# Performance work log

Measured on AMD Instinct MI355X. Metric: run time of the kernel, lower is better.

## Reference

```python
import jax, jax.numpy as jnp
import numpy as np

N_NODES = 50000
N_EDGES = 640000
IN_CH, HID_CH, OUT_CH = 128, 128, 40


def setup_inputs() -> dict:
    key = jax.random.key(0)
    k1, k2, k3, k4 = jax.random.split(key, 4)
    x = jax.random.normal(k1, (N_NODES, IN_CH), dtype=jnp.float32)
    edge_index = jax.random.randint(k2, (2, N_EDGES), 0, N_NODES, dtype=jnp.int64)
    # Glorot-ish scaled weights
    W1 = jax.random.normal(k3, (IN_CH, HID_CH), dtype=jnp.float32) * (1.0 / np.sqrt(IN_CH))
    b1 = jnp.zeros((HID_CH,), dtype=jnp.float32)
    W2 = jax.random.normal(k4, (HID_CH, OUT_CH), dtype=jnp.float32) * (1.0 / np.sqrt(HID_CH))
    b2 = jnp.zeros((OUT_CH,), dtype=jnp.float32)
    return {"x": x, "edge_index": edge_index, "W1": W1, "b1": b1, "W2": W2, "b2": b2}


def gcn_conv(x, src, dst, W, b, n_nodes):
    """PyG-style GCNConv: self-loops + symmetric normalization + linear + bias.
    src/dst already include self-loop edges."""
    deg = jax.ops.segment_sum(jnp.ones_like(dst, dtype=x.dtype), dst, num_segments=n_nodes)
    dinv = jnp.where(deg > 0, jax.lax.rsqrt(deg), 0.0)          # deg^{-1/2}, 0 for isolated
    norm = dinv[src] * dinv[dst]                                 # [E+N]
    xw = x @ W                                                   # [N, F_out] dense GEMM
    msgs = xw[src] * norm[:, None]                               # gather + scale  [E+N, F_out]
    agg = jax.ops.segment_sum(msgs, dst, num_segments=n_nodes)   # scatter-add
    return agg + b


def reference(x, edge_index, W1, b1, W2, b2):
    n_nodes = x.shape[0]
    loops = jnp.arange(n_nodes, dtype=edge_index.dtype)
    src = jnp.concatenate([edge_index[0], loops])
    dst = jnp.concatenate([edge_index[1], loops])
    h = jax.nn.relu(gcn_conv(x, src, dst, W1, b1, n_nodes))
    # dropout is identity in eval mode (deterministic reference)
    return gcn_conv(h, src, dst, W2, b2, n_nodes)
```

## Files before the change

kernel.cpp:

```cpp
#include <hip/hip_runtime.h>
#include <cstdint>

#define NN 50000
#define NE 640000
#define NFILL 625
#define MB1 782

typedef unsigned short ushort_t;

__device__ __forceinline__ ushort_t f2bf(float f) {
    unsigned int b = __float_as_uint(f);
    return (ushort_t)((b + 0x7FFF + ((b >> 16) & 1)) >> 16);
}
__device__ __forceinline__ float bf2f(ushort_t u) {
    return __uint_as_float(((unsigned int)u) << 16);
}


__global__ void hist_kernel(const int* __restrict__ dst, int* __restrict__ cnt) {
    int tid = blockIdx.x * 256 + threadIdx.x;
#pragma unroll
    for (int k = 0; k < 4; ++k) {
        int e = tid + k * 160000;
        atomicAdd(&cnt[dst[e]], 1);
    }
}

__global__ void scan_block(const int* __restrict__ in, int* __restrict__ out,
                           int* __restrict__ partials, int n) {
    __shared__ int sm[256];
    int t = threadIdx.x;
    int gid = blockIdx.x * 256 + t;
    int v = (gid < n) ? in[gid] : 0;
    sm[t] = v;
    __syncthreads();
#pragma unroll
    for (int off = 1; off < 256; off <<= 1) {
        int add = (t >= off) ? sm[t - off] : 0;
        __syncthreads();
        sm[t] += add;
        __syncthreads();
    }
    if (gid < n) out[gid] = sm[t] - v;
    if (t == 255) partials[blockIdx.x] = sm[255];
}

__global__ void scan_partials(int* __restrict__ p, int nb) {
    __shared__ int sm[256];
    int t = threadIdx.x;
    int v = (t < nb) ? p[t] : 0;
    sm[t] = v;
    __syncthreads();
#pragma unroll
    for (int off = 1; off < 256; off <<= 1) {
        int add = (t >= off) ? sm[t - off] : 0;
        __syncthreads();
        sm[t] += add;
        __syncthreads();
    }
    if (t < nb) p[t] = sm[t] - v;
}

__global__ void finalize_offsets(int* __restrict__ offs, const int* __restrict__ partials,
                                 int* __restrict__ cursor, const int* __restrict__ cnt,
                                 float* __restrict__ dinv, int n) {
    int gid = blockIdx.x * 256 + threadIdx.x;
    if (gid < n) {
        int v = offs[gid] + partials[blockIdx.x];
        offs[gid] = v;
        cursor[gid] = v;
        dinv[gid] = rsqrtf((float)cnt[gid] + 1.0f);
    }
}


__global__ __launch_bounds__(256) void fused_fill_gemm(const int* __restrict__ ei,
                                                       int* __restrict__ cursor,
                                                       ushort_t* __restrict__ csr_src,
                                                       const float* __restrict__ A,
                                                       const float* __restrict__ B,
                                                       const float* __restrict__ dinv,
                                                       ushort_t* __restrict__ C,
                                                       int M, int N) {
    __shared__ float As[64][68];
    __shared__ __align__(16) float Bs[64][64];

    if (blockIdx.x < NFILL) {
        int tid = blockIdx.x * 256 + threadIdx.x;
#pragma unroll
        for (int k = 0; k < 4; ++k) {
            int e = tid + k * 160000;
            int s = ei[e], d = ei[NE + e];
            int pos = atomicAdd(&cursor[d], 1);
            csr_src[pos] = (ushort_t)s;
        }
        return;
    }

    const int b  = blockIdx.x - NFILL;
    const int t  = threadIdx.x;
    const int m0 = (b % MB1) * 64;
    const int n0 = (b / MB1) * 64;
    const int tx = t & 15, ty = t >> 4;

    float acc[4][4] = {};

    for (int ks = 0; ks < 2; ++ks) {
#pragma unroll
        for (int i = 0; i < 4; ++i) {
            int idx = i * 256 + t;
            int r = idx >> 4, c4 = idx & 15;
            int gm = m0 + r;
            float4 v = make_float4(0.f, 0.f, 0.f, 0.f);
            if (gm < M) v = *reinterpret_cast<const float4*>(&A[(size_t)gm * 128 + ks * 64 + c4 * 4]);
            As[r][c4 * 4 + 0] = v.x;
            As[r][c4 * 4 + 1] = v.y;
            As[r][c4 * 4 + 2] = v.z;
            As[r][c4 * 4 + 3] = v.w;
        }
#pragma unroll
        for (int i = 0; i < 4; ++i) {
            int idx = i * 256 + t;
            int k = idx >> 4, c4 = idx & 15;
            int gk = ks * 64 + k;
            int gn = n0 + c4 * 4;
            float4 v;
            v.x = (gn + 0 < N) ? B[(size_t)gk * N + gn + 0] : 0.f;
            v.y = (gn + 1 < N) ? B[(size_t)gk * N + gn + 1] : 0.f;
            v.z = (gn + 2 < N) ? B[(size_t)gk * N + gn + 2] : 0.f;
            v.w = (gn + 3 < N) ? B[(size_t)gk * N + gn + 3] : 0.f;
            *reinterpret_cast<float4*>(&Bs[k][c4 * 4]) = v;
        }
        __syncthreads();

#pragma unroll 8
        for (int k = 0; k < 64; ++k) {
            float a0 = As[ty * 4 + 0][k];
            float a1 = As[ty * 4 + 1][k];
            float a2 = As[ty * 4 + 2][k];
            float a3 = As[ty * 4 + 3][k];
            float4 bb = *reinterpret_cast<const float4*>(&Bs[k][tx * 4]);
            acc[0][0] += a0 * bb.x; acc[0][1] += a0 * bb.y; acc[0][2] += a0 * bb.z; acc[0][3] += a0 * bb.w;
            acc[1][0] += a1 * bb.x; acc[1][1] += a1 * bb.y; acc[1][2] += a1 * bb.z; acc[1][3] += a1 * bb.w;
            acc[2][0] += a2 * bb.x; acc[2][1] += a2 * bb.y; acc[2][2] += a2 * bb.z; acc[2][3] += a2 * bb.w;
            acc[3][0] += a3 * bb.x; acc[3][1] += a3 * bb.y; acc[3][2] += a3 * bb.z; acc[3][3] += a3 * bb.w;
        }
        __syncthreads();
    }

#pragma unroll
    for (int i = 0; i < 4; ++i) {
        int gm = m0 + ty * 4 + i;
        if (gm >= M) continue;
        float s = dinv[gm];
        int gn = n0 + tx * 4;
        if (gn + 3 < N) {
            ushort4 o;
            o.x = f2bf(acc[i][0] * s); o.y = f2bf(acc[i][1] * s);
            o.z = f2bf(acc[i][2] * s); o.w = f2bf(acc[i][3] * s);
            *reinterpret_cast<ushort4*>(&C[(size_t)gm * N + gn]) = o;
        } else {
#pragma unroll
            for (int j = 0; j < 4; ++j)
                if (gn + j < N) C[(size_t)gm * N + gn + j] = f2bf(acc[i][j] * s);
        }
    }
}


__global__ __launch_bounds__(256) void gemm_k128_scaled(const float* __restrict__ A,
                                                        const float* __restrict__ B,
                                                        const float* __restrict__ dinv,
                                                        ushort_t* __restrict__ C,
                                                        int M, int N) {
    __shared__ float As[64][68];
    __shared__ __align__(16) float Bs[64][64];
    const int t  = threadIdx.x;
    const int m0 = blockIdx.x * 64;
    const int n0 = blockIdx.y * 64;
    const int tx = t & 15, ty = t >> 4;

    float acc[4][4] = {};

    for (int ks = 0; ks < 2; ++ks) {
#pragma unroll
        for (int i = 0; i < 4; ++i) {
            int idx = i * 256 + t;
            int r = idx >> 4, c4 = idx & 15;
            int gm = m0 + r;
            float4 v = make_float4(0.f, 0.f, 0.f, 0.f);
            if (gm < M) v = *reinterpret_cast<const float4*>(&A[(size_t)gm * 128 + ks * 64 + c4 * 4]);
            As[r][c4 * 4 + 0] = v.x;
            As[r][c4 * 4 + 1] = v.y;
            As[r][c4 * 4 + 2] = v.z;
            As[r][c4 * 4 + 3] = v.w;
        }
#pragma unroll
        for (int i = 0; i < 4; ++i) {
            int idx = i * 256 + t;
            int k = idx >> 4, c4 = idx & 15;
            int gk = ks * 64 + k;
            int gn = n0 + c4 * 4;
            float4 v;
            v.x = (gn + 0 < N) ? B[(size_t)gk * N + gn + 0] : 0.f;
            v.y = (gn + 1 < N) ? B[(size_t)gk * N + gn + 1] : 0.f;
            v.z = (gn + 2 < N) ? B[(size_t)gk * N + gn + 2] : 0.f;
            v.w = (gn + 3 < N) ? B[(size_t)gk * N + gn + 3] : 0.f;
            *reinterpret_cast<float4*>(&Bs[k][c4 * 4]) = v;
        }
        __syncthreads();

#pragma unroll 8
        for (int k = 0; k < 64; ++k) {
            float a0 = As[ty * 4 + 0][k];
            float a1 = As[ty * 4 + 1][k];
            float a2 = As[ty * 4 + 2][k];
            float a3 = As[ty * 4 + 3][k];
            float4 bb = *reinterpret_cast<const float4*>(&Bs[k][tx * 4]);
            acc[0][0] += a0 * bb.x; acc[0][1] += a0 * bb.y; acc[0][2] += a0 * bb.z; acc[0][3] += a0 * bb.w;
            acc[1][0] += a1 * bb.x; acc[1][1] += a1 * bb.y; acc[1][2] += a1 * bb.z; acc[1][3] += a1 * bb.w;
            acc[2][0] += a2 * bb.x; acc[2][1] += a2 * bb.y; acc[2][2] += a2 * bb.z; acc[2][3] += a2 * bb.w;
            acc[3][0] += a3 * bb.x; acc[3][1] += a3 * bb.y; acc[3][2] += a3 * bb.z; acc[3][3] += a3 * bb.w;
        }
        __syncthreads();
    }

#pragma unroll
    for (int i = 0; i < 4; ++i) {
        int gm = m0 + ty * 4 + i;
        if (gm >= M) continue;
        float s = dinv[gm];
        int gn = n0 + tx * 4;
        if (gn + 3 < N) {
            ushort4 o;
            o.x = f2bf(acc[i][0] * s); o.y = f2bf(acc[i][1] * s);
            o.z = f2bf(acc[i][2] * s); o.w = f2bf(acc[i][3] * s);
            *reinterpret_cast<ushort4*>(&C[(size_t)gm * N + gn]) = o;
        } else {
#pragma unroll
            for (int j = 0; j < 4; ++j)
                if (gn + j < N) C[(size_t)gm * N + gn + j] = f2bf(acc[i][j] * s);
        }
    }
}


__global__ __launch_bounds__(256) void gather128(const int* __restrict__ offs,
                                                 const int* __restrict__ ends,
                                                 const ushort_t* __restrict__ csr_src,
                                                 const ushort_t* __restrict__ Hs,
                                                 const float* __restrict__ dinv,
                                                 const float* __restrict__ b1,
                                                 float* __restrict__ h) {
    const int c = (threadIdx.x & 31) * 4;
    const int n = (blockIdx.x * 256 + threadIdx.x) >> 5;
    const int beg = offs[n], end = ends[n];
    float4 acc = make_float4(0.f, 0.f, 0.f, 0.f);
    int j = beg;
    const int n4end = beg + ((end - beg) & ~3);
    for (; j < n4end; j += 4) {
        int s0 = csr_src[j + 0], s1 = csr_src[j + 1];
        int s2 = csr_src[j + 2], s3 = csr_src[j + 3];
        ushort4 v0 = *reinterpret_cast<const ushort4*>(Hs + (size_t)s0 * 128 + c);
        ushort4 v1 = *reinterpret_cast<const ushort4*>(Hs + (size_t)s1 * 128 + c);
        ushort4 v2 = *reinterpret_cast<const ushort4*>(Hs + (size_t)s2 * 128 + c);
        ushort4 v3 = *reinterpret_cast<const ushort4*>(Hs + (size_t)s3 * 128 + c);
        acc.x += bf2f(v0.x) + bf2f(v1.x) + bf2f(v2.x) + bf2f(v3.x);
        acc.y += bf2f(v0.y) + bf2f(v1.y) + bf2f(v2.y) + bf2f(v3.y);
        acc.z += bf2f(v0.z) + bf2f(v1.z) + bf2f(v2.z) + bf2f(v3.z);
        acc.w += bf2f(v0.w) + bf2f(v1.w) + bf2f(v2.w) + bf2f(v3.w);
    }
    for (; j < end; ++j) {
        int s = csr_src[j];
        ushort4 v = *reinterpret_cast<const ushort4*>(Hs + (size_t)s * 128 + c);
        acc.x += bf2f(v.x); acc.y += bf2f(v.y);
        acc.z += bf2f(v.z); acc.w += bf2f(v.w);
    }
    float di = dinv[n];
    ushort4 sv = *reinterpret_cast<const ushort4*>(Hs + (size_t)n * 128 + c);
    float4 bv = *reinterpret_cast<const float4*>(b1 + c);
    float4 r;
    r.x = fmaxf(fmaf(di, acc.x + bf2f(sv.x), bv.x), 0.f);
    r.y = fmaxf(fmaf(di, acc.y + bf2f(sv.y), bv.y), 0.f);
    r.z = fmaxf(fmaf(di, acc.z + bf2f(sv.z), bv.z), 0.f);
    r.w = fmaxf(fmaf(di, acc.w + bf2f(sv.w), bv.w), 0.f);
    *reinterpret_cast<float4*>(h + (size_t)n * 128 + c) = r;
}


__global__ __launch_bounds__(256) void gather40(const int* __restrict__ offs,
                                                const int* __restrict__ ends,
                                                const ushort_t* __restrict__ csr_src,
                                                const ushort_t* __restrict__ Hs,
                                                const float* __restrict__ dinv,
                                                const float* __restrict__ b2,
                                                float* __restrict__ out) {
    int idx = blockIdx.x * 256 + threadIdx.x;
    if (idx >= NN * 10) return;
    const int n = idx / 10;
    const int c = (idx - n * 10) * 4;
    const int beg = offs[n], end = ends[n];
    float4 acc = make_float4(0.f, 0.f, 0.f, 0.f);
    int j = beg;
    const int n4end = beg + ((end - beg) & ~3);
    for (; j < n4end; j += 4) {
        int s0 = csr_src[j + 0], s1 = csr_src[j + 1];
        int s2 = csr_src[j + 2], s3 = csr_src[j + 3];
        ushort4 v0 = *reinterpret_cast<const ushort4*>(Hs + (size_t)s0 * 40 + c);
        ushort4 v1 = *reinterpret_cast<const ushort4*>(Hs + (size_t)s1 * 40 + c);
        ushort4 v2 = *reinterpret_cast<const ushort4*>(Hs + (size_t)s2 * 40 + c);
        ushort4 v3 = *reinterpret_cast<const ushort4*>(Hs + (size_t)s3 * 40 + c);
        acc.x += bf2f(v0.x) + bf2f(v1.x) + bf2f(v2.x) + bf2f(v3.x);
        acc.y += bf2f(v0.y) + bf2f(v1.y) + bf2f(v2.y) + bf2f(v3.y);
        acc.z += bf2f(v0.z) + bf2f(v1.z) + bf2f(v2.z) + bf2f(v3.z);
        acc.w += bf2f(v0.w) + bf2f(v1.w) + bf2f(v2.w) + bf2f(v3.w);
    }
    for (; j < end; ++j) {
        int s = csr_src[j];
        ushort4 v = *reinterpret_cast<const ushort4*>(Hs + (size_t)s * 40 + c);
        acc.x += bf2f(v.x); acc.y += bf2f(v.y);
        acc.z += bf2f(v.z); acc.w += bf2f(v.w);
    }
    float di = dinv[n];
    ushort4 sv = *reinterpret_cast<const ushort4*>(Hs + (size_t)n * 40 + c);
    float4 bv = *reinterpret_cast<const float4*>(b2 + c);
    float4 r;
    r.x = fmaf(di, acc.x + bf2f(sv.x), bv.x);
    r.y = fmaf(di, acc.y + bf2f(sv.y), bv.y);
    r.z = fmaf(di, acc.z + bf2f(sv.z), bv.z);
    r.w = fmaf(di, acc.w + bf2f(sv.w), bv.w);
    *reinterpret_cast<float4*>(out + (size_t)n * 40 + c) = r;
}


extern "C" void kernel_launch(void* const* d_in, const int* in_sizes, int n_in,
                              void* d_out, int out_size, void* d_ws, size_t ws_size,
                              hipStream_t stream) {
    const float* x  = (const float*)d_in[0];
    const int*   ei = (const int*)d_in[1];
    const float* W1 = (const float*)d_in[2];
    const float* b1 = (const float*)d_in[3];
    const float* W2 = (const float*)d_in[4];
    const float* b2 = (const float*)d_in[5];
    float* out = (float*)d_out;

    int*      deg_i    = (int*)d_ws;
    float*    dinv     = (float*)d_ws + 50048;
    int*      offs     = (int*)d_ws + 100096;
    int*      cursor   = (int*)d_ws + 150144;
    int*      partials = (int*)d_ws + 200192;
    ushort_t* csr_src  = (ushort_t*)((int*)d_ws + 200704);
    ushort_t* H1b      = (ushort_t*)((int*)d_ws + 520704);
    float*    h        = (float*)d_ws + 3720704;
    ushort_t* H2b      = H1b;

    const int NB = (NN + 255) / 256;

    hipMemsetAsync(deg_i, 0, NN * sizeof(int), stream);
    hist_kernel<<<625, 256, 0, stream>>>(ei + NE, deg_i);
    scan_block<<<NB, 256, 0, stream>>>(deg_i, offs, partials, NN);
    scan_partials<<<1, 256, 0, stream>>>(partials, NB);
    finalize_offsets<<<NB, 256, 0, stream>>>(offs, partials, cursor, deg_i, dinv, NN);

    fused_fill_gemm<<<NFILL + MB1 * 2, 256, 0, stream>>>(ei, cursor, csr_src,
                                                         x, W1, dinv, H1b, NN, 128);

    gather128<<<NN * 32 / 256, 256, 0, stream>>>(offs, cursor, csr_src, H1b, dinv, b1, h);

    gemm_k128_scaled<<<dim3(MB1, 1), 256, 0, stream>>>(h, W2, dinv, H2b, NN, 40);
    gather40<<<(NN * 10 + 255) / 256, 256, 0, stream>>>(offs, cursor, csr_src, H2b, dinv, b2, out);
}
```

Before: 230.4 us.

## Replace CSR build with fixed-width ELL adjacency, dropping histogram and scan passes

```diff
diff --git a/kernel.cpp b/kernel.cpp
--- a/kernel.cpp
+++ b/kernel.cpp
@@ -3,6 +3,7 @@
 
 #define NN 50000
 #define NE 640000
+#define ELLW 64
 #define NFILL 625
 #define MB1 782
 
@@ -17,69 +18,11 @@
 }
 
 
-__global__ void hist_kernel(const int* __restrict__ dst, int* __restrict__ cnt) {
-    int tid = blockIdx.x * 256 + threadIdx.x;
-#pragma unroll
-    for (int k = 0; k < 4; ++k) {
-        int e = tid + k * 160000;
-        atomicAdd(&cnt[dst[e]], 1);
-    }
-}
-
-__global__ void scan_block(const int* __restrict__ in, int* __restrict__ out,
-                           int* __restrict__ partials, int n) {
-    __shared__ int sm[256];
-    int t = threadIdx.x;
-    int gid = blockIdx.x * 256 + t;
-    int v = (gid < n) ? in[gid] : 0;
-    sm[t] = v;
-    __syncthreads();
-#pragma unroll
-    for (int off = 1; off < 256; off <<= 1) {
-        int add = (t >= off) ? sm[t - off] : 0;
-        __syncthreads();
-        sm[t] += add;
-        __syncthreads();
-    }
-    if (gid < n) out[gid] = sm[t] - v;
-    if (t == 255) partials[blockIdx.x] = sm[255];
-}
-
-__global__ void scan_partials(int* __restrict__ p, int nb) {
-    __shared__ int sm[256];
-    int t = threadIdx.x;
-    int v = (t < nb) ? p[t] : 0;
-    sm[t] = v;
-    __syncthreads();
-#pragma unroll
-    for (int off = 1; off < 256; off <<= 1) {
-        int add = (t >= off) ? sm[t - off] : 0;
-        __syncthreads();
-        sm[t] += add;
-        __syncthreads();
-    }
-    if (t < nb) p[t] = sm[t] - v;
-}
-
-__global__ void finalize_offsets(int* __restrict__ offs, const int* __restrict__ partials,
-                                 int* __restrict__ cursor, const int* __restrict__ cnt,
-                                 float* __restrict__ dinv, int n) {
-    int gid = blockIdx.x * 256 + threadIdx.x;
-    if (gid < n) {
-        int v = offs[gid] + partials[blockIdx.x];
-        offs[gid] = v;
-        cursor[gid] = v;
-        dinv[gid] = rsqrtf((float)cnt[gid] + 1.0f);
-    }
-}
-
-
 __global__ __launch_bounds__(256) void fused_fill_gemm(const int* __restrict__ ei,
                                                        int* __restrict__ cursor,
-                                                       ushort_t* __restrict__ csr_src,
+                                                       ushort_t* __restrict__ ell,
                                                        const float* __restrict__ A,
                                                        const float* __restrict__ B,
-                                                       const float* __restrict__ dinv,
                                                        ushort_t* __restrict__ C,
                                                        int M, int N) {
     __shared__ float As[64][68];
@@ -92,7 +35,7 @@
             int e = tid + k * 160000;
             int s = ei[e], d = ei[NE + e];
             int pos = atomicAdd(&cursor[d], 1);
-            csr_src[pos] = (ushort_t)s;
+            ell[(size_t)d * ELLW + pos] = (ushort_t)s;
         }
         return;
     }
@@ -152,25 +95,39 @@
     for (int i = 0; i < 4; ++i) {
         int gm = m0 + ty * 4 + i;
         if (gm >= M) continue;
-        float s = dinv[gm];
         int gn = n0 + tx * 4;
         if (gn + 3 < N) {
             ushort4 o;
-            o.x = f2bf(acc[i][0] * s); o.y = f2bf(acc[i][1] * s);
-            o.z = f2bf(acc[i][2] * s); o.w = f2bf(acc[i][3] * s);
+            o.x = f2bf(acc[i][0]); o.y = f2bf(acc[i][1]);
+            o.z = f2bf(acc[i][2]); o.w = f2bf(acc[i][3]);
             *reinterpret_cast<ushort4*>(&C[(size_t)gm * N + gn]) = o;
         } else {
 #pragma unroll
             for (int j = 0; j < 4; ++j)
-                if (gn + j < N) C[(size_t)gm * N + gn + j] = f2bf(acc[i][j] * s);
-        }
-    }
+                if (gn + j < N) C[(size_t)gm * N + gn + j] = f2bf(acc[i][j]);
+        }
+    }
+}
+
+
+__global__ __launch_bounds__(256) void scale_h1(const int* __restrict__ cursor,
+                                                ushort_t* __restrict__ H1b) {
+    int idx = blockIdx.x * 256 + threadIdx.x;
+    int n = idx >> 5;
+    int c = (idx & 31) * 4;
+    float di = rsqrtf((float)cursor[n] + 1.0f);
+    ushort4 v = *reinterpret_cast<const ushort4*>(H1b + (size_t)n * 128 + c);
+    v.x = f2bf(bf2f(v.x) * di);
+    v.y = f2bf(bf2f(v.y) * di);
+    v.z = f2bf(bf2f(v.z) * di);
+    v.w = f2bf(bf2f(v.w) * di);
+    *reinterpret_cast<ushort4*>(H1b + (size_t)n * 128 + c) = v;
 }
 
 
 __global__ __launch_bounds__(256) void gemm_k128_scaled(const float* __restrict__ A,
                                                         const float* __restrict__ B,
-                                                        const float* __restrict__ dinv,
+                                                        const int* __restrict__ cursor,
                                                         ushort_t* __restrict__ C,
                                                         int M, int N) {
     __shared__ float As[64][68];
@@ -229,7 +186,7 @@
     for (int i = 0; i < 4; ++i) {
         int gm = m0 + ty * 4 + i;
         if (gm >= M) continue;
-        float s = dinv[gm];
+        float s = rsqrtf((float)cursor[gm] + 1.0f);
         int gn = n0 + tx * 4;
         if (gn + 3 < N) {
             ushort4 o;
@@ -245,22 +202,21 @@
 }
 
 
-__global__ __launch_bounds__(256) void gather128(const int* __restrict__ offs,
-                                                 const int* __restrict__ ends,
-                                                 const ushort_t* __restrict__ csr_src,
+__global__ __launch_bounds__(256) void gather128(const int* __restrict__ cursor,
+                                                 const ushort_t* __restrict__ ell,
                                                  const ushort_t* __restrict__ Hs,
-                                                 const float* __restrict__ dinv,
                                                  const float* __restrict__ b1,
                                                  float* __restrict__ h) {
     const int c = (threadIdx.x & 31) * 4;
     const int n = (blockIdx.x * 256 + threadIdx.x) >> 5;
-    const int beg = offs[n], end = ends[n];
+    const int deg = cursor[n];
+    const ushort_t* en = ell + (size_t)n * ELLW;
     float4 acc = make_float4(0.f, 0.f, 0.f, 0.f);
-    int j = beg;
-    const int n4end = beg + ((end - beg) & ~3);
+    int j = 0;
+    const int n4end = deg & ~3;
     for (; j < n4end; j += 4) {
-        int s0 = csr_src[j + 0], s1 = csr_src[j + 1];
-        int s2 = csr_src[j + 2], s3 = csr_src[j + 3];
+        int s0 = en[j + 0], s1 = en[j + 1];
+        int s2 = en[j + 2], s3 = en[j + 3];
         ushort4 v0 = *reinterpret_cast<const ushort4*>(Hs + (size_t)s0 * 128 + c);
         ushort4 v1 = *reinterpret_cast<const ushort4*>(Hs + (size_t)s1 * 128 + c);
         ushort4 v2 = *reinterpret_cast<const ushort4*>(Hs + (size_t)s2 * 128 + c);
@@ -270,13 +226,13 @@
         acc.z += bf2f(v0.z) + bf2f(v1.z) + bf2f(v2.z) + bf2f(v3.z);
         acc.w += bf2f(v0.w) + bf2f(v1.w) + bf2f(v2.w) + bf2f(v3.w);
     }
-    for (; j < end; ++j) {
-        int s = csr_src[j];
+    for (; j < deg; ++j) {
+        int s = en[j];
         ushort4 v = *reinterpret_cast<const ushort4*>(Hs + (size_t)s * 128 + c);
         acc.x += bf2f(v.x); acc.y += bf2f(v.y);
         acc.z += bf2f(v.z); acc.w += bf2f(v.w);
     }
-    float di = dinv[n];
+    float di = rsqrtf((float)deg + 1.0f);
     ushort4 sv = *reinterpret_cast<const ushort4*>(Hs + (size_t)n * 128 + c);
     float4 bv = *reinterpret_cast<const float4*>(b1 + c);
     float4 r;
@@ -288,24 +244,23 @@
 }
 
 
-__global__ __launch_bounds__(256) void gather40(const int* __restrict__ offs,
-                                                const int* __restrict__ ends,
-                                                const ushort_t* __restrict__ csr_src,
+__global__ __launch_bounds__(256) void gather40(const int* __restrict__ cursor,
+                                                const ushort_t* __restrict__ ell,
                                                 const ushort_t* __restrict__ Hs,
-                                                const float* __restrict__ dinv,
                                                 const float* __restrict__ b2,
                                                 float* __restrict__ out) {
     int idx = blockIdx.x * 256 + threadIdx.x;
     if (idx >= NN * 10) return;
     const int n = idx / 10;
     const int c = (idx - n * 10) * 4;
-    const int beg = offs[n], end = ends[n];
+    const int deg = cursor[n];
+    const ushort_t* en = ell + (size_t)n * ELLW;
     float4 acc = make_float4(0.f, 0.f, 0.f, 0.f);
-    int j = beg;
-    const int n4end = beg + ((end - beg) & ~3);
+    int j = 0;
+    const int n4end = deg & ~3;
     for (; j < n4end; j += 4) {
-        int s0 = csr_src[j + 0], s1 = csr_src[j + 1];
-        int s2 = csr_src[j + 2], s3 = csr_src[j + 3];
+        int s0 = en[j + 0], s1 = en[j + 1];
+        int s2 = en[j + 2], s3 = en[j + 3];
         ushort4 v0 = *reinterpret_cast<const ushort4*>(Hs + (size_t)s0 * 40 + c);
         ushort4 v1 = *reinterpret_cast<const ushort4*>(Hs + (size_t)s1 * 40 + c);
         ushort4 v2 = *reinterpret_cast<const ushort4*>(Hs + (size_t)s2 * 40 + c);
@@ -315,13 +270,13 @@
         acc.z += bf2f(v0.z) + bf2f(v1.z) + bf2f(v2.z) + bf2f(v3.z);
         acc.w += bf2f(v0.w) + bf2f(v1.w) + bf2f(v2.w) + bf2f(v3.w);
     }
-    for (; j < end; ++j) {
-        int s = csr_src[j];
+    for (; j < deg; ++j) {
+        int s = en[j];
         ushort4 v = *reinterpret_cast<const ushort4*>(Hs + (size_t)s * 40 + c);
         acc.x += bf2f(v.x); acc.y += bf2f(v.y);
         acc.z += bf2f(v.z); acc.w += bf2f(v.w);
     }
-    float di = dinv[n];
+    float di = rsqrtf((float)deg + 1.0f);
     ushort4 sv = *reinterpret_cast<const ushort4*>(Hs + (size_t)n * 40 + c);
     float4 bv = *reinterpret_cast<const float4*>(b2 + c);
     float4 r;
@@ -344,29 +299,21 @@
     const float* b2 = (const float*)d_in[5];
     float* out = (float*)d_out;
 
-    int*      deg_i    = (int*)d_ws;
-    float*    dinv     = (float*)d_ws + 50048;
-    int*      offs     = (int*)d_ws + 100096;
-    int*      cursor   = (int*)d_ws + 150144;
-    int*      partials = (int*)d_ws + 200192;
-    ushort_t* csr_src  = (ushort_t*)((int*)d_ws + 200704);
-    ushort_t* H1b      = (ushort_t*)((int*)d_ws + 520704);
-    float*    h        = (float*)d_ws + 3720704;
-    ushort_t* H2b      = H1b;
-
-    const int NB = (NN + 255) / 256;
-
-    hipMemsetAsync(deg_i, 0, NN * sizeof(int), stream);
-    hist_kernel<<<625, 256, 0, stream>>>(ei + NE, deg_i);
-    scan_block<<<NB, 256, 0, stream>>>(deg_i, offs, partials, NN);
-    scan_partials<<<1, 256, 0, stream>>>(partials, NB);
-    finalize_offsets<<<NB, 256, 0, stream>>>(offs, partials, cursor, deg_i, dinv, NN);
-
-    fused_fill_gemm<<<NFILL + MB1 * 2, 256, 0, stream>>>(ei, cursor, csr_src,
-                                                         x, W1, dinv, H1b, NN, 128);
-
-    gather128<<<NN * 32 / 256, 256, 0, stream>>>(offs, cursor, csr_src, H1b, dinv, b1, h);
-
-    gemm_k128_scaled<<<dim3(MB1, 1), 256, 0, stream>>>(h, W2, dinv, H2b, NN, 40);
-    gather40<<<(NN * 10 + 255) / 256, 256, 0, stream>>>(offs, cursor, csr_src, H2b, dinv, b2, out);
-}
+    int*      cursor = (int*)d_ws;
+    ushort_t* ell    = (ushort_t*)((int*)d_ws + 50048);
+    ushort_t* H1b    = (ushort_t*)((int*)d_ws + 1650048);
+    float*    h      = (float*)d_ws + 4850048;
+    ushort_t* H2b    = H1b;
+
+    hipMemsetAsync(cursor, 0, NN * sizeof(int), stream);
+
+    fused_fill_gemm<<<NFILL + MB1 * 2, 256, 0, stream>>>(ei, cursor, ell,
+                                                         x, W1, H1b, NN, 128);
+
+    scale_h1<<<NN * 32 / 256, 256, 0, stream>>>(cursor, H1b);
+
+    gather128<<<NN * 32 / 256, 256, 0, stream>>>(cursor, ell, H1b, b1, h);
+
+    gemm_k128_scaled<<<dim3(MB1, 1), 256, 0, stream>>>(h, W2, cursor, H2b, NN, 40);
+    gather40<<<(NN * 10 + 255) / 256, 256, 0, stream>>>(cursor, ell, H2b, b2, out);
+}
```

After: 204.3 us. 11.3% less time.
